# Optimization experiments

Measured on AMD Instinct MI355X. Metric: run time of the kernel, lower is better.

Reference implementation:

```python
import jax, jax.numpy as jnp
import numpy as np

N_NODES = 50000
N_GRAPHS = 64
D = 320


def gcn_conv(x, W, b, src, dst, n):
    # PyG GCNConv (default): add self loops, symmetric deg^-1/2 normalization,
    # linear transform, scatter-add aggregation at target, plus bias.
    h = x @ W  # [N, d_out]
    loop = jnp.arange(n)
    s = jnp.concatenate([src, loop])
    t = jnp.concatenate([dst, loop])
    deg = jax.ops.segment_sum(jnp.ones_like(t, dtype=h.dtype), t, num_segments=n)
    dinv = jnp.where(deg > 0, jax.lax.rsqrt(deg), 0.0)
    norm = dinv[s] * dinv[t]  # [E+N]
    msg = h[s] * norm[:, None]  # gather + scale, [E+N, d_out]
    out = jax.ops.segment_sum(msg, t, num_segments=n)
    return out + b


def setup_inputs() -> dict:
    key = jax.random.key(0)
    ks = jax.random.split(key, 12)
    x = jax.random.normal(ks[0], (N_NODES, D), dtype=jnp.float32)
    edge_index = jax.random.randint(ks[1], (2, 800000), 0, N_NODES, dtype=jnp.int64)
    batch = jnp.sort(jax.random.randint(ks[2], (N_NODES,), 0, N_GRAPHS, dtype=jnp.int64))

    def lin(k, fan_in, fan_out):
        bound = 1.0 / np.sqrt(fan_in)
        kw, kb = jax.random.split(k)
        W = jax.random.uniform(kw, (fan_in, fan_out), minval=-bound, maxval=bound, dtype=jnp.float32)
        b = jax.random.uniform(kb, (fan_out,), minval=-bound, maxval=bound, dtype=jnp.float32)
        return W, b

    W1, b1 = lin(ks[3], D, D)
    W2, b2 = lin(ks[4], D, D)
    W3, b3 = lin(ks[5], D, D)
    Wf1, bf1 = lin(ks[6], D, 256)
    Wf2, bf2 = lin(ks[7], 256, 16)
    Wf3, bf3 = lin(ks[8], 16, 1)
    return {"x": x, "W1": W1, "b1": b1, "W2": W2, "b2": b2, "W3": W3, "b3": b3,
            "Wf1": Wf1, "bf1": bf1, "Wf2": Wf2, "bf2": bf2, "Wf3": Wf3, "bf3": bf3,
            "edge_index": edge_index, "batch": batch}


def reference(x, W1, b1, W2, b2, W3, b3, Wf1, bf1, Wf2, bf2, Wf3, bf3, edge_index, batch):
    src, dst = edge_index[0], edge_index[1]
    n = x.shape[0]
    h = jax.nn.relu(gcn_conv(x, W1, b1, src, dst, n))
    h = jax.nn.relu(gcn_conv(h, W2, b2, src, dst, n))
    h = jax.nn.relu(gcn_conv(h, W3, b3, src, dst, n))
    g = jax.ops.segment_max(h, batch, num_segments=N_GRAPHS)  # global max pool [B, D]
    g = jax.nn.relu(g @ Wf1 + bf1)  # dropout is identity in eval mode
    g = jax.nn.relu(g @ Wf2 + bf2)
    return g @ Wf3 + bf3
```

## Files before the change

kernel.cpp:

```cpp
#include <hip/hip_runtime.h>
#include <hip/hip_bf16.h>

#define N_NODES 50000
#define N_EDGES 800000
#define N_GRAPHS 64
#define D 320
#define CAP 64
#define POOL_SPLIT 4

typedef __attribute__((ext_vector_type(8))) short s16x8;
typedef __attribute__((ext_vector_type(4))) float f32x4;
typedef __attribute__((ext_vector_type(4))) unsigned int u32x4;

__device__ inline ushort f2bf(float f) {
    __hip_bfloat16 h = __float2bfloat16(f);
    return *reinterpret_cast<ushort*>(&h);
}

__global__ __launch_bounds__(256) void k_cvt_w3(const float* __restrict__ W1,
                                                const float* __restrict__ W2,
                                                const float* __restrict__ W3,
                                                ushort* __restrict__ Wt) {
    int i = blockIdx.x * blockDim.x + threadIdx.x;
    if (i >= 3 * D * D) return;
    int w = i / (D * D), r = i % (D * D);
    const float* W = (w == 0) ? W1 : (w == 1) ? W2 : W3;
    int k = r / D, n = r % D;
    Wt[w * D * D + n * D + k] = f2bf(W[r]);
}

__global__ void k_fill(const int* __restrict__ src, const int* __restrict__ dst,
                       int* __restrict__ cursor, int* __restrict__ csr) {
    int e = blockIdx.x * blockDim.x + threadIdx.x;
    if (e < N_EDGES) {
        int d = dst[e];
        int p = atomicAdd(&cursor[d], 1);
        if (p < CAP) csr[d * CAP + p] = src[e];
    }
}

__global__ void k_dinv(const int* __restrict__ cursor, float* __restrict__ dinv) {
    int n = blockIdx.x * blockDim.x + threadIdx.x;
    if (n < N_NODES) dinv[n] = rsqrtf((float)(cursor[n] + 1));
}

#define GBM 128
#define GBK 32
#define LDK 40
template<int AMODE>
__global__ __launch_bounds__(512) void k_gemm(const void* __restrict__ Ain,
                                              const ushort* __restrict__ Wt,
                                              const float* __restrict__ dinv,
                                              ushort* __restrict__ P) {
    __shared__ ushort As[GBM][LDK];
    __shared__ ushort Bs[D][LDK];
    int t = threadIdx.x;
    int m0 = blockIdx.x * GBM;
    int lane = t & 63;
    int wid = t >> 6;
    int wm = wid & 1;
    int wn = wid >> 1;
    int r16 = lane & 15;
    int kb = (lane >> 4) * 8;

    f32x4 acc[4][5] = {};

    for (int k0 = 0; k0 < D; k0 += GBK) {
        #pragma unroll
        for (int u = 0; u < 4; ++u) {
            int gi = t + 512 * u;
            if (gi < 512) {
                int r = gi >> 2, s = gi & 3;
                int gr = m0 + r;
                s16x8 v = {};
                if (gr < N_NODES) {
                    int k = k0 + s * 8;
                    if constexpr (AMODE == 1) {
                        const float* Af = (const float*)Ain;
                        float4 a0 = *(const float4*)&Af[(size_t)gr * D + k];
                        float4 a1 = *(const float4*)&Af[(size_t)gr * D + k + 4];
                        v[0] = (short)f2bf(a0.x); v[1] = (short)f2bf(a0.y);
                        v[2] = (short)f2bf(a0.z); v[3] = (short)f2bf(a0.w);
                        v[4] = (short)f2bf(a1.x); v[5] = (short)f2bf(a1.y);
                        v[6] = (short)f2bf(a1.z); v[7] = (short)f2bf(a1.w);
                    } else {
                        const ushort* Ab = (const ushort*)Ain;
                        v = *(const s16x8*)&Ab[(size_t)gr * D + k];
                    }
                }
                *(s16x8*)&As[r][s * 8] = v;
            } else if (gi < 1792) {
                int gj = gi - 512;
                int r = gj >> 2, s = gj & 3;
                *(s16x8*)&Bs[r][s * 8] = *(const s16x8*)&Wt[(size_t)r * D + k0 + s * 8];
            }
        }
        __syncthreads();

        s16x8 af[4], bfr[5];
        #pragma unroll
        for (int mi = 0; mi < 4; ++mi)
            af[mi] = *(const s16x8*)&As[wm * 64 + mi * 16 + r16][kb];
        #pragma unroll
        for (int ni = 0; ni < 5; ++ni)
            bfr[ni] = *(const s16x8*)&Bs[wn * 80 + ni * 16 + r16][kb];
        #pragma unroll
        for (int mi = 0; mi < 4; ++mi)
            #pragma unroll
            for (int ni = 0; ni < 5; ++ni)
                acc[mi][ni] = __builtin_amdgcn_mfma_f32_16x16x32_bf16(af[mi], bfr[ni], acc[mi][ni], 0, 0, 0);
        __syncthreads();
    }

    #pragma unroll
    for (int mi = 0; mi < 4; ++mi) {
        int rbase = m0 + wm * 64 + mi * 16 + (lane >> 4) * 4;
        #pragma unroll
        for (int r = 0; r < 4; ++r) {
            int row = rbase + r;
            if (row < N_NODES) {
                float dv = dinv[row];
                #pragma unroll
                for (int ni = 0; ni < 5; ++ni) {
                    int col = wn * 80 + ni * 16 + r16;
                    P[(size_t)row * D + col] = f2bf(acc[mi][ni][r] * dv);
                }
            }
        }
    }
}

#define AGG_NPB 8
__global__ __launch_bounds__(320) void k_agg(const ushort* __restrict__ P,
                                             const int* __restrict__ cursor,
                                             const int* __restrict__ csr,
                                             const float* __restrict__ dinv,
                                             const float* __restrict__ bias,
                                             ushort* __restrict__ H) {
    int t = threadIdx.x;
    int nl = t / 40;
    int cg = t - nl * 40;
    int n  = blockIdx.x * AGG_NPB + nl;
    int c0 = cg * 8;
    size_t row = (size_t)n * D + c0;
    const char* Pb = (const char*)P;
    unsigned coff = (unsigned)(c0 * 2);

    f32x4 aE = {}, aO = {};
    {
        u32x4 u = *(const u32x4*)&P[row];
        aE += __builtin_bit_cast(f32x4, u << 16);
        aO += __builtin_bit_cast(f32x4, u & (unsigned int)0xffff0000u);
    }
    int deg = cursor[n];
    if (deg > CAP) deg = CAP;
    const int* lst = csr + n * CAP;
    int i = 0;
    for (; i + 4 <= deg; i += 4) {
        int s0 = lst[i], s1 = lst[i + 1], s2 = lst[i + 2], s3 = lst[i + 3];
        u32x4 u0 = *(const u32x4*)(Pb + (unsigned)s0 * (unsigned)(D * 2) + coff);
        u32x4 u1 = *(const u32x4*)(Pb + (unsigned)s1 * (unsigned)(D * 2) + coff);
        u32x4 u2 = *(const u32x4*)(Pb + (unsigned)s2 * (unsigned)(D * 2) + coff);
        u32x4 u3 = *(const u32x4*)(Pb + (unsigned)s3 * (unsigned)(D * 2) + coff);
        aE += __builtin_bit_cast(f32x4, u0 << 16);
        aO += __builtin_bit_cast(f32x4, u0 & (unsigned int)0xffff0000u);
        aE += __builtin_bit_cast(f32x4, u1 << 16);
        aO += __builtin_bit_cast(f32x4, u1 & (unsigned int)0xffff0000u);
        aE += __builtin_bit_cast(f32x4, u2 << 16);
        aO += __builtin_bit_cast(f32x4, u2 & (unsigned int)0xffff0000u);
        aE += __builtin_bit_cast(f32x4, u3 << 16);
        aO += __builtin_bit_cast(f32x4, u3 & (unsigned int)0xffff0000u);
    }
    for (; i < deg; ++i) {
        int s = lst[i];
        u32x4 u = *(const u32x4*)(Pb + (unsigned)s * (unsigned)(D * 2) + coff);
        aE += __builtin_bit_cast(f32x4, u << 16);
        aO += __builtin_bit_cast(f32x4, u & (unsigned int)0xffff0000u);
    }
    float dv = dinv[n];
    s16x8 ov;
    #pragma unroll
    for (int q = 0; q < 4; ++q) {
        float e = fmaxf(fmaf(dv, aE[q], bias[c0 + 2 * q]), 0.0f);
        float o = fmaxf(fmaf(dv, aO[q], bias[c0 + 2 * q + 1]), 0.0f);
        ov[2 * q]     = (short)f2bf(e);
        ov[2 * q + 1] = (short)f2bf(o);
    }
    *(s16x8*)&H[row] = ov;
}

__global__ __launch_bounds__(320) void k_pool(const ushort* __restrict__ H,
                                              const int* __restrict__ batch,
                                              float* __restrict__ Gp) {
    __shared__ int range[2];
    int sp = blockIdx.x;
    int b = blockIdx.y;
    int t = threadIdx.x;
    int nl = t / 40;
    int cg = t - nl * 40;
    int c0 = cg * 8;
    if (t < 2) {
        int target = b + t;
        int lo = 0, hi = N_NODES;
        while (lo < hi) {
            int mid = (lo + hi) >> 1;
            if (batch[mid] < target) lo = mid + 1; else hi = mid;
        }
        range[t] = lo;
    }
    __syncthreads();
    int s = range[0], e = range[1];
    f32x4 mE = {}, mO = {};
    for (int n = s + sp * 8 + nl; n < e; n += POOL_SPLIT * 8) {
        u32x4 u = *(const u32x4*)&H[(size_t)n * D + c0];
        f32x4 vE = __builtin_bit_cast(f32x4, u << 16);
        f32x4 vO = __builtin_bit_cast(f32x4, u & (unsigned int)0xffff0000u);
        #pragma unroll
        for (int q = 0; q < 4; ++q) {
            mE[q] = fmaxf(mE[q], vE[q]);
            mO[q] = fmaxf(mO[q], vO[q]);
        }
    }
    __shared__ float red[8][D];
    #pragma unroll
    for (int q = 0; q < 4; ++q) {
        red[nl][c0 + 2 * q]     = mE[q];
        red[nl][c0 + 2 * q + 1] = mO[q];
    }
    __syncthreads();
    if (nl == 0) {
        #pragma unroll
        for (int q = 0; q < 8; ++q) {
            int c = c0 + q;
            float m = red[0][c];
            #pragma unroll
            for (int r = 1; r < 8; ++r) m = fmaxf(m, red[r][c]);
            Gp[(sp * N_GRAPHS + b) * D + c] = m;
        }
    }
}

__global__ __launch_bounds__(256) void k_mlp(const float* __restrict__ Gp,
    const float* __restrict__ Wf1, const float* __restrict__ bf1,
    const float* __restrict__ Wf2, const float* __restrict__ bf2,
    const float* __restrict__ Wf3, const float* __restrict__ bf3,
    float* __restrict__ out) {
    __shared__ float g_s[D];
    __shared__ float s1[256];
    __shared__ float s2[16];
    int b = blockIdx.x;
    int t = threadIdx.x;
    for (int i = t; i < D; i += 256) {
        float m = Gp[b * D + i];
        #pragma unroll
        for (int sp = 1; sp < POOL_SPLIT; ++sp)
            m = fmaxf(m, Gp[(sp * N_GRAPHS + b) * D + i]);
        g_s[i] = m;
    }
    __syncthreads();
    float acc = bf1[t];
    for (int k = 0; k < D; ++k) acc = fmaf(g_s[k], Wf1[k * 256 + t], acc);
    s1[t] = fmaxf(acc, 0.0f);
    __syncthreads();
    if (t < 16) {
        float a2 = bf2[t];
        for (int k = 0; k < 256; ++k) a2 = fmaf(s1[k], Wf2[k * 16 + t], a2);
        s2[t] = fmaxf(a2, 0.0f);
    }
    __syncthreads();
    if (t == 0) {
        float a3 = bf3[0];
        #pragma unroll
        for (int k = 0; k < 16; ++k) a3 = fmaf(s2[k], Wf3[k], a3);
        out[b] = a3;
    }
}

extern "C" void kernel_launch(void* const* d_in, const int* in_sizes, int n_in,
                              void* d_out, int out_size, void* d_ws, size_t ws_size,
                              hipStream_t stream) {
    const float* x   = (const float*)d_in[0];
    const float* W1  = (const float*)d_in[1];
    const float* b1  = (const float*)d_in[2];
    const float* W2  = (const float*)d_in[3];
    const float* b2  = (const float*)d_in[4];
    const float* W3  = (const float*)d_in[5];
    const float* b3  = (const float*)d_in[6];
    const float* Wf1 = (const float*)d_in[7];
    const float* bf1 = (const float*)d_in[8];
    const float* Wf2 = (const float*)d_in[9];
    const float* bf2 = (const float*)d_in[10];
    const float* Wf3 = (const float*)d_in[11];
    const float* bf3 = (const float*)d_in[12];
    const int*   ei  = (const int*)d_in[13];
    const int*   src = ei;
    const int*   dst = ei + N_EDGES;
    const int*   batch = (const int*)d_in[14];
    float* out = (float*)d_out;

    char* p = (char*)d_ws;
    auto alloc = [&](size_t bytes) { char* r = p; p += (bytes + 255) & ~(size_t)255; return (void*)r; };
    const size_t NB = (size_t)N_NODES * D * sizeof(ushort);
    ushort* bB   = (ushort*)alloc(NB);
    ushort* bC   = (ushort*)alloc(NB);
    ushort* Wt   = (ushort*)alloc(3 * D * D * 2);
    float*  dinv = (float*)alloc(N_NODES * 4);
    int*    cursor = (int*)alloc(N_NODES * 4);
    int*    csr  = (int*)alloc((size_t)N_NODES * CAP * 4);
    float*  Gp   = (float*)alloc(POOL_SPLIT * N_GRAPHS * D * 4);

    hipMemsetAsync(cursor, 0, N_NODES * sizeof(int), stream);

    k_cvt_w3<<<(3 * D * D + 255) / 256, 256, 0, stream>>>(W1, W2, W3, Wt);

    k_fill<<<(N_EDGES + 255) / 256, 256, 0, stream>>>(src, dst, cursor, csr);
    k_dinv<<<(N_NODES + 255) / 256, 256, 0, stream>>>(cursor, dinv);

    int ggrid = (N_NODES + GBM - 1) / GBM;
    int agrid = N_NODES / AGG_NPB;
    k_gemm<1><<<ggrid, 512, 0, stream>>>(x, Wt, dinv, bB);
    k_agg<<<agrid, 320, 0, stream>>>(bB, cursor, csr, dinv, b1, bC);
    k_gemm<0><<<ggrid, 512, 0, stream>>>(bC, Wt + D * D, dinv, bB);
    k_agg<<<agrid, 320, 0, stream>>>(bB, cursor, csr, dinv, b2, bC);
    k_gemm<0><<<ggrid, 512, 0, stream>>>(bC, Wt + 2 * D * D, dinv, bB);
    k_agg<<<agrid, 320, 0, stream>>>(bB, cursor, csr, dinv, b3, bC);
    dim3 pgrid(POOL_SPLIT, N_GRAPHS);
    k_pool<<<pgrid, 320, 0, stream>>>(bC, batch, Gp);
    k_mlp<<<N_GRAPHS, 256, 0, stream>>>(Gp, Wf1, bf1, Wf2, bf2, Wf3, bf3, out);
}
```

Measured before the change: 395.0 us.

## Use direct global-to-LDS loads with XOR-style swizzle and fold dinv into consumers

The GEMM now loads the A (bf16 layers) and W tiles straight from global memory into LDS through global_load_lds, placed in a rotated-slot swizzle in place of padded rows. This removes the register round-trip and should avoid LDS bank conflicts. The separate dinv kernel and buffer are removed, and rsqrt(deg+1) is recomputed from cursor inside the GEMM epilogue and the aggregation kernel. The activation buffers are padded by one tile of rows so the unguarded direct loads past N_NODES stay in bounds, at the cost of reading garbage rows that are never stored.

```diff
diff --git a/kernel.cpp b/kernel.cpp
--- a/kernel.cpp
+++ b/kernel.cpp
@@ -15,6 +15,12 @@
 __device__ inline ushort f2bf(float f) {
     __hip_bfloat16 h = __float2bfloat16(f);
     return *reinterpret_cast<ushort*>(&h);
+}
+
+__device__ __forceinline__ void gload16(const void* g, void* l) {
+    __builtin_amdgcn_global_load_lds(
+        (const __attribute__((address_space(1))) unsigned int*)g,
+        (__attribute__((address_space(3))) unsigned int*)l, 16, 0, 0);
 }
 
 __global__ __launch_bounds__(256) void k_cvt_w3(const float* __restrict__ W1,
@@ -39,71 +45,74 @@
     }
 }
 
-__global__ void k_dinv(const int* __restrict__ cursor, float* __restrict__ dinv) {
-    int n = blockIdx.x * blockDim.x + threadIdx.x;
-    if (n < N_NODES) dinv[n] = rsqrtf((float)(cursor[n] + 1));
-}
-
 #define GBM 128
 #define GBK 32
-#define LDK 40
 template<int AMODE>
 __global__ __launch_bounds__(512) void k_gemm(const void* __restrict__ Ain,
                                               const ushort* __restrict__ Wt,
-                                              const float* __restrict__ dinv,
+                                              const int* __restrict__ cursor,
                                               ushort* __restrict__ P) {
-    __shared__ ushort As[GBM][LDK];
-    __shared__ ushort Bs[D][LDK];
+    __shared__ ushort As[GBM][GBK];
+    __shared__ ushort Bs[D][GBK];
     int t = threadIdx.x;
+    int lane = t & 63;
+    int w = t >> 6;
     int m0 = blockIdx.x * GBM;
-    int lane = t & 63;
-    int wid = t >> 6;
-    int wm = wid & 1;
-    int wn = wid >> 1;
+    int wm = w & 1;
+    int wn = w >> 1;
     int r16 = lane & 15;
-    int kb = (lane >> 4) * 8;
+    int tseg = lane >> 4;
+    int physsel = (tseg + (r16 >> 1)) & 3;
+
+    int agi = w * 64 + lane;
+    int ar = agi >> 2;
+    int asl = ((agi & 3) - (agi >> 3)) & 3;
+    char* AsWaveBase = (char*)As + w * 1024;
 
     f32x4 acc[4][5] = {};
 
     for (int k0 = 0; k0 < D; k0 += GBK) {
-        #pragma unroll
-        for (int u = 0; u < 4; ++u) {
-            int gi = t + 512 * u;
-            if (gi < 512) {
-                int r = gi >> 2, s = gi & 3;
-                int gr = m0 + r;
-                s16x8 v = {};
-                if (gr < N_NODES) {
-                    int k = k0 + s * 8;
-                    if constexpr (AMODE == 1) {
-                        const float* Af = (const float*)Ain;
-                        float4 a0 = *(const float4*)&Af[(size_t)gr * D + k];
-                        float4 a1 = *(const float4*)&Af[(size_t)gr * D + k + 4];
-                        v[0] = (short)f2bf(a0.x); v[1] = (short)f2bf(a0.y);
-                        v[2] = (short)f2bf(a0.z); v[3] = (short)f2bf(a0.w);
-                        v[4] = (short)f2bf(a1.x); v[5] = (short)f2bf(a1.y);
-                        v[6] = (short)f2bf(a1.z); v[7] = (short)f2bf(a1.w);
-                    } else {
-                        const ushort* Ab = (const ushort*)Ain;
-                        v = *(const s16x8*)&Ab[(size_t)gr * D + k];
-                    }
-                }
-                *(s16x8*)&As[r][s * 8] = v;
-            } else if (gi < 1792) {
-                int gj = gi - 512;
-                int r = gj >> 2, s = gj & 3;
-                *(s16x8*)&Bs[r][s * 8] = *(const s16x8*)&Wt[(size_t)r * D + k0 + s * 8];
+        if constexpr (AMODE == 0) {
+            const char* Ab = (const char*)Ain;
+            gload16(Ab + ((size_t)(m0 + ar) * D + k0 + asl * 8) * 2, AsWaveBase);
+        } else {
+            int gr = m0 + ar;
+            s16x8 v = {};
+            if (gr < N_NODES) {
+                const float* Af = (const float*)Ain;
+                const float* srcp = &Af[(size_t)gr * D + k0 + asl * 8];
+                float4 a0 = *(const float4*)srcp;
+                float4 a1 = *(const float4*)(srcp + 4);
+                v[0] = (short)f2bf(a0.x); v[1] = (short)f2bf(a0.y);
+                v[2] = (short)f2bf(a0.z); v[3] = (short)f2bf(a0.w);
+                v[4] = (short)f2bf(a1.x); v[5] = (short)f2bf(a1.y);
+                v[6] = (short)f2bf(a1.z); v[7] = (short)f2bf(a1.w);
             }
+            *(s16x8*)((char*)As + (size_t)agi * 16) = v;
+        }
+        #pragma unroll
+        for (int u = 0; u < 3; ++u) {
+            int gi = u * 512 + t;
+            if (gi < 1280) {
+                int r = gi >> 2;
+                int sl = ((gi & 3) - (gi >> 3)) & 3;
+                gload16((const char*)Wt + (size_t)r * (D * 2) + (size_t)(k0 + sl * 8) * 2,
+                        (char*)Bs + (size_t)(u * 512 + (t & ~63)) * 16);
+            }
         }
         __syncthreads();
 
         s16x8 af[4], bfr[5];
         #pragma unroll
-        for (int mi = 0; mi < 4; ++mi)
-            af[mi] = *(const s16x8*)&As[wm * 64 + mi * 16 + r16][kb];
-        #pragma unroll
-        for (int ni = 0; ni < 5; ++ni)
-            bfr[ni] = *(const s16x8*)&Bs[wn * 80 + ni * 16 + r16][kb];
+        for (int mi = 0; mi < 4; ++mi) {
+            int row = wm * 64 + mi * 16 + r16;
+            af[mi] = *(const s16x8*)((const char*)As + (size_t)row * 64 + physsel * 16);
+        }
+        #pragma unroll
+        for (int ni = 0; ni < 5; ++ni) {
+            int row = wn * 80 + ni * 16 + r16;
+            bfr[ni] = *(const s16x8*)((const char*)Bs + (size_t)row * 64 + physsel * 16);
+        }
         #pragma unroll
         for (int mi = 0; mi < 4; ++mi)
             #pragma unroll
@@ -119,7 +128,7 @@
         for (int r = 0; r < 4; ++r) {
             int row = rbase + r;
             if (row < N_NODES) {
-                float dv = dinv[row];
+                float dv = rsqrtf((float)(cursor[row] + 1));
                 #pragma unroll
                 for (int ni = 0; ni < 5; ++ni) {
                     int col = wn * 80 + ni * 16 + r16;
@@ -134,7 +143,6 @@
 __global__ __launch_bounds__(320) void k_agg(const ushort* __restrict__ P,
                                              const int* __restrict__ cursor,
                                              const int* __restrict__ csr,
-                                             const float* __restrict__ dinv,
                                              const float* __restrict__ bias,
                                              ushort* __restrict__ H) {
     int t = threadIdx.x;
@@ -152,8 +160,8 @@
         aE += __builtin_bit_cast(f32x4, u << 16);
         aO += __builtin_bit_cast(f32x4, u & (unsigned int)0xffff0000u);
     }
-    int deg = cursor[n];
-    if (deg > CAP) deg = CAP;
+    int cnt = cursor[n];
+    int deg = cnt > CAP ? CAP : cnt;
     const int* lst = csr + n * CAP;
     int i = 0;
     for (; i + 4 <= deg; i += 4) {
@@ -177,7 +185,7 @@
         aE += __builtin_bit_cast(f32x4, u << 16);
         aO += __builtin_bit_cast(f32x4, u & (unsigned int)0xffff0000u);
     }
-    float dv = dinv[n];
+    float dv = rsqrtf((float)(cnt + 1));
     s16x8 ov;
     #pragma unroll
     for (int q = 0; q < 4; ++q) {
@@ -300,11 +308,10 @@
 
     char* p = (char*)d_ws;
     auto alloc = [&](size_t bytes) { char* r = p; p += (bytes + 255) & ~(size_t)255; return (void*)r; };
-    const size_t NB = (size_t)N_NODES * D * sizeof(ushort);
-    ushort* bB   = (ushort*)alloc(NB);
-    ushort* bC   = (ushort*)alloc(NB);
+    const size_t NBP = (size_t)(N_NODES + GBM) * D * sizeof(ushort);
+    ushort* bB   = (ushort*)alloc(NBP);
+    ushort* bC   = (ushort*)alloc(NBP);
     ushort* Wt   = (ushort*)alloc(3 * D * D * 2);
-    float*  dinv = (float*)alloc(N_NODES * 4);
     int*    cursor = (int*)alloc(N_NODES * 4);
     int*    csr  = (int*)alloc((size_t)N_NODES * CAP * 4);
     float*  Gp   = (float*)alloc(POOL_SPLIT * N_GRAPHS * D * 4);
@@ -314,16 +321,15 @@
     k_cvt_w3<<<(3 * D * D + 255) / 256, 256, 0, stream>>>(W1, W2, W3, Wt);
 
     k_fill<<<(N_EDGES + 255) / 256, 256, 0, stream>>>(src, dst, cursor, csr);
-    k_dinv<<<(N_NODES + 255) / 256, 256, 0, stream>>>(cursor, dinv);
 
     int ggrid = (N_NODES + GBM - 1) / GBM;
     int agrid = N_NODES / AGG_NPB;
-    k_gemm<1><<<ggrid, 512, 0, stream>>>(x, Wt, dinv, bB);
-    k_agg<<<agrid, 320, 0, stream>>>(bB, cursor, csr, dinv, b1, bC);
-    k_gemm<0><<<ggrid, 512, 0, stream>>>(bC, Wt + D * D, dinv, bB);
-    k_agg<<<agrid, 320, 0, stream>>>(bB, cursor, csr, dinv, b2, bC);
-    k_gemm<0><<<ggrid, 512, 0, stream>>>(bC, Wt + 2 * D * D, dinv, bB);
-    k_agg<<<agrid, 320, 0, stream>>>(bB, cursor, csr, dinv, b3, bC);
+    k_gemm<1><<<ggrid, 512, 0, stream>>>(x, Wt, cursor, bB);
+    k_agg<<<agrid, 320, 0, stream>>>(bB, cursor, csr, b1, bC);
+    k_gemm<0><<<ggrid, 512, 0, stream>>>(bC, Wt + D * D, cursor, bB);
+    k_agg<<<agrid, 320, 0, stream>>>(bB, cursor, csr, b2, bC);
+    k_gemm<0><<<ggrid, 512, 0, stream>>>(bC, Wt + 2 * D * D, cursor, bB);
+    k_agg<<<agrid, 320, 0, stream>>>(bB, cursor, csr, b3, bC);
     dim3 pgrid(POOL_SPLIT, N_GRAPHS);
     k_pool<<<pgrid, 320, 0, stream>>>(bC, batch, Gp);
     k_mlp<<<N_GRAPHS, 256, 0, stream>>>(Gp, Wf1, bf1, Wf2, bf2, Wf3, bf3, out);
```

After: 406.0 us. +2.8%, slower.

## Fuse max-pool into last aggregation and fold memset and dinv into other kernels

Applied to the files above, without the earlier changes.

The global max pool now happens inside the final aggregation kernel. Each block reduces its 8 nodes per graph segment in shared memory and applies atomicMax on float bits to a zeroed G buffer, so the final H write and the separate pool kernel are no longer needed. The memset of cursor and the dinv kernel are removed: zeroing moves into the weight-conversion kernel, and rsqrt of the degree is recomputed inline in the gemm and aggregation kernels. This cuts launches and one full pass over H. The cost is atomic traffic, and the int atomicMax trick is valid only because post-ReLU values are non-negative.

```diff
diff --git a/kernel.cpp b/kernel.cpp
--- a/kernel.cpp
+++ b/kernel.cpp
@@ -6,7 +6,6 @@
 #define N_GRAPHS 64
 #define D 320
 #define CAP 64
-#define POOL_SPLIT 4
 
 typedef __attribute__((ext_vector_type(8))) short s16x8;
 typedef __attribute__((ext_vector_type(4))) float f32x4;
@@ -17,16 +16,21 @@
     return *reinterpret_cast<ushort*>(&h);
 }
 
-__global__ __launch_bounds__(256) void k_cvt_w3(const float* __restrict__ W1,
-                                                const float* __restrict__ W2,
-                                                const float* __restrict__ W3,
-                                                ushort* __restrict__ Wt) {
+__global__ __launch_bounds__(256) void k_prep(const float* __restrict__ W1,
+                                              const float* __restrict__ W2,
+                                              const float* __restrict__ W3,
+                                              ushort* __restrict__ Wt,
+                                              int* __restrict__ cursor,
+                                              float* __restrict__ G) {
     int i = blockIdx.x * blockDim.x + threadIdx.x;
-    if (i >= 3 * D * D) return;
-    int w = i / (D * D), r = i % (D * D);
-    const float* W = (w == 0) ? W1 : (w == 1) ? W2 : W3;
-    int k = r / D, n = r % D;
-    Wt[w * D * D + n * D + k] = f2bf(W[r]);
+    if (i < N_NODES) cursor[i] = 0;
+    if (i < N_GRAPHS * D) G[i] = 0.0f;
+    if (i < 3 * D * D) {
+        int w = i / (D * D), r = i % (D * D);
+        const float* W = (w == 0) ? W1 : (w == 1) ? W2 : W3;
+        int k = r / D, n = r % D;
+        Wt[w * D * D + n * D + k] = f2bf(W[r]);
+    }
 }
 
 __global__ void k_fill(const int* __restrict__ src, const int* __restrict__ dst,
@@ -39,18 +43,13 @@
     }
 }
 
-__global__ void k_dinv(const int* __restrict__ cursor, float* __restrict__ dinv) {
-    int n = blockIdx.x * blockDim.x + threadIdx.x;
-    if (n < N_NODES) dinv[n] = rsqrtf((float)(cursor[n] + 1));
-}
-
 #define GBM 128
 #define GBK 32
 #define LDK 40
 template<int AMODE>
 __global__ __launch_bounds__(512) void k_gemm(const void* __restrict__ Ain,
                                               const ushort* __restrict__ Wt,
-                                              const float* __restrict__ dinv,
+                                              const int* __restrict__ cursor,
                                               ushort* __restrict__ P) {
     __shared__ ushort As[GBM][LDK];
     __shared__ ushort Bs[D][LDK];
@@ -119,7 +118,7 @@
         for (int r = 0; r < 4; ++r) {
             int row = rbase + r;
             if (row < N_NODES) {
-                float dv = dinv[row];
+                float dv = rsqrtf((float)(cursor[row] + 1));
                 #pragma unroll
                 for (int ni = 0; ni < 5; ++ni) {
                     int col = wn * 80 + ni * 16 + r16;
@@ -131,12 +130,16 @@
 }
 
 #define AGG_NPB 8
+template<int POOL>
 __global__ __launch_bounds__(320) void k_agg(const ushort* __restrict__ P,
                                              const int* __restrict__ cursor,
                                              const int* __restrict__ csr,
-                                             const float* __restrict__ dinv,
                                              const float* __restrict__ bias,
-                                             ushort* __restrict__ H) {
+                                             ushort* __restrict__ H,
+                                             const int* __restrict__ batch,
+                                             float* __restrict__ G) {
+    __shared__ float red[AGG_NPB][D];
+    __shared__ int gid[AGG_NPB];
     int t = threadIdx.x;
     int nl = t / 40;
     int cg = t - nl * 40;
@@ -146,14 +149,16 @@
     const char* Pb = (const char*)P;
     unsigned coff = (unsigned)(c0 * 2);
 
+    if (POOL && t < AGG_NPB) gid[t] = (int)batch[blockIdx.x * AGG_NPB + t];
+
     f32x4 aE = {}, aO = {};
     {
         u32x4 u = *(const u32x4*)&P[row];
         aE += __builtin_bit_cast(f32x4, u << 16);
         aO += __builtin_bit_cast(f32x4, u & (unsigned int)0xffff0000u);
     }
-    int deg = cursor[n];
-    if (deg > CAP) deg = CAP;
+    int cnt = cursor[n];
+    int deg = cnt > CAP ? CAP : cnt;
     const int* lst = csr + n * CAP;
     int i = 0;
     for (; i + 4 <= deg; i += 4) {
@@ -177,70 +182,47 @@
         aE += __builtin_bit_cast(f32x4, u << 16);
         aO += __builtin_bit_cast(f32x4, u & (unsigned int)0xffff0000u);
     }
-    float dv = dinv[n];
-    s16x8 ov;
-    #pragma unroll
-    for (int q = 0; q < 4; ++q) {
-        float e = fmaxf(fmaf(dv, aE[q], bias[c0 + 2 * q]), 0.0f);
-        float o = fmaxf(fmaf(dv, aO[q], bias[c0 + 2 * q + 1]), 0.0f);
-        ov[2 * q]     = (short)f2bf(e);
-        ov[2 * q + 1] = (short)f2bf(o);
-    }
-    *(s16x8*)&H[row] = ov;
-}
-
-__global__ __launch_bounds__(320) void k_pool(const ushort* __restrict__ H,
-                                              const int* __restrict__ batch,
-                                              float* __restrict__ Gp) {
-    __shared__ int range[2];
-    int sp = blockIdx.x;
-    int b = blockIdx.y;
-    int t = threadIdx.x;
-    int nl = t / 40;
-    int cg = t - nl * 40;
-    int c0 = cg * 8;
-    if (t < 2) {
-        int target = b + t;
-        int lo = 0, hi = N_NODES;
-        while (lo < hi) {
-            int mid = (lo + hi) >> 1;
-            if (batch[mid] < target) lo = mid + 1; else hi = mid;
-        }
-        range[t] = lo;
-    }
-    __syncthreads();
-    int s = range[0], e = range[1];
-    f32x4 mE = {}, mO = {};
-    for (int n = s + sp * 8 + nl; n < e; n += POOL_SPLIT * 8) {
-        u32x4 u = *(const u32x4*)&H[(size_t)n * D + c0];
-        f32x4 vE = __builtin_bit_cast(f32x4, u << 16);
-        f32x4 vO = __builtin_bit_cast(f32x4, u & (unsigned int)0xffff0000u);
+    float dv = rsqrtf((float)(cnt + 1));
+
+    if constexpr (POOL == 0) {
+        s16x8 ov;
         #pragma unroll
         for (int q = 0; q < 4; ++q) {
-            mE[q] = fmaxf(mE[q], vE[q]);
-            mO[q] = fmaxf(mO[q], vO[q]);
-        }
-    }
-    __shared__ float red[8][D];
-    #pragma unroll
-    for (int q = 0; q < 4; ++q) {
-        red[nl][c0 + 2 * q]     = mE[q];
-        red[nl][c0 + 2 * q + 1] = mO[q];
-    }
-    __syncthreads();
-    if (nl == 0) {
-        #pragma unroll
-        for (int q = 0; q < 8; ++q) {
-            int c = c0 + q;
-            float m = red[0][c];
+            float e = fmaxf(fmaf(dv, aE[q], bias[c0 + 2 * q]), 0.0f);
+            float o = fmaxf(fmaf(dv, aO[q], bias[c0 + 2 * q + 1]), 0.0f);
+            ov[2 * q]     = (short)f2bf(e);
+            ov[2 * q + 1] = (short)f2bf(o);
+        }
+        *(s16x8*)&H[row] = ov;
+    } else {
+        #pragma unroll
+        for (int q = 0; q < 4; ++q) {
+            red[nl][c0 + 2 * q]     = fmaxf(fmaf(dv, aE[q], bias[c0 + 2 * q]), 0.0f);
+            red[nl][c0 + 2 * q + 1] = fmaxf(fmaf(dv, aO[q], bias[c0 + 2 * q + 1]), 0.0f);
+        }
+        __syncthreads();
+        if (nl == 0) {
             #pragma unroll
-            for (int r = 1; r < 8; ++r) m = fmaxf(m, red[r][c]);
-            Gp[(sp * N_GRAPHS + b) * D + c] = m;
-        }
-    }
-}
-
-__global__ __launch_bounds__(256) void k_mlp(const float* __restrict__ Gp,
+            for (int q = 0; q < 8; ++q) {
+                int c = c0 + q;
+                float m = red[0][c];
+                int g = gid[0];
+                #pragma unroll
+                for (int r = 1; r < AGG_NPB; ++r) {
+                    if (gid[r] == g) m = fmaxf(m, red[r][c]);
+                    else {
+                        atomicMax((int*)&G[g * D + c], __float_as_int(m));
+                        g = gid[r];
+                        m = red[r][c];
+                    }
+                }
+                atomicMax((int*)&G[g * D + c], __float_as_int(m));
+            }
+        }
+    }
+}
+
+__global__ __launch_bounds__(256) void k_mlp(const float* __restrict__ G,
     const float* __restrict__ Wf1, const float* __restrict__ bf1,
     const float* __restrict__ Wf2, const float* __restrict__ bf2,
     const float* __restrict__ Wf3, const float* __restrict__ bf3,
@@ -250,13 +232,7 @@
     __shared__ float s2[16];
     int b = blockIdx.x;
     int t = threadIdx.x;
-    for (int i = t; i < D; i += 256) {
-        float m = Gp[b * D + i];
-        #pragma unroll
-        for (int sp = 1; sp < POOL_SPLIT; ++sp)
-            m = fmaxf(m, Gp[(sp * N_GRAPHS + b) * D + i]);
-        g_s[i] = m;
-    }
+    for (int i = t; i < D; i += 256) g_s[i] = G[b * D + i];
     __syncthreads();
     float acc = bf1[t];
     for (int k = 0; k < D; ++k) acc = fmaf(g_s[k], Wf1[k * 256 + t], acc);
@@ -304,27 +280,20 @@
     ushort* bB   = (ushort*)alloc(NB);
     ushort* bC   = (ushort*)alloc(NB);
     ushort* Wt   = (ushort*)alloc(3 * D * D * 2);
-    float*  dinv = (float*)alloc(N_NODES * 4);
     int*    cursor = (int*)alloc(N_NODES * 4);
     int*    csr  = (int*)alloc((size_t)N_NODES * CAP * 4);
-    float*  Gp   = (float*)alloc(POOL_SPLIT * N_GRAPHS * D * 4);
-
-    hipMemsetAsync(cursor, 0, N_NODES * sizeof(int), stream);
-
-    k_cvt_w3<<<(3 * D * D + 255) / 256, 256, 0, stream>>>(W1, W2, W3, Wt);
-
+    float*  G    = (float*)alloc(N_GRAPHS * D * 4);
+
+    k_prep<<<(3 * D * D + 255) / 256, 256, 0, stream>>>(W1, W2, W3, Wt, cursor, G);
     k_fill<<<(N_EDGES + 255) / 256, 256, 0, stream>>>(src, dst, cursor, csr);
-    k_dinv<<<(N_NODES + 255) / 256, 256, 0, stream>>>(cursor, dinv);
 
     int ggrid = (N_NODES + GBM - 1) / GBM;
     int agrid = N_NODES / AGG_NPB;
-    k_gemm<1><<<ggrid, 512, 0, stream>>>(x, Wt, dinv, bB);
-    k_agg<<<agrid, 320, 0, stream>>>(bB, cursor, csr, dinv, b1, bC);
-    k_gemm<0><<<ggrid, 512, 0, stream>>>(bC, Wt + D * D, dinv, bB);
-    k_agg<<<agrid, 320, 0, stream>>>(bB, cursor, csr, dinv, b2, bC);
-    k_gemm<0><<<ggrid, 512, 0, stream>>>(bC, Wt + 2 * D * D, dinv, bB);
-    k_agg<<<agrid, 320, 0, stream>>>(bB, cursor, csr, dinv, b3, bC);
-    dim3 pgrid(POOL_SPLIT, N_GRAPHS);
-    k_pool<<<pgrid, 320, 0, stream>>>(bC, batch, Gp);
-    k_mlp<<<N_GRAPHS, 256, 0, stream>>>(Gp, Wf1, bf1, Wf2, bf2, Wf3, bf3, out);
-}
+    k_gemm<1><<<ggrid, 512, 0, stream>>>(x, Wt, cursor, bB);
+    k_agg<0><<<agrid, 320, 0, stream>>>(bB, cursor, csr, b1, bC, nullptr, nullptr);
+    k_gemm<0><<<ggrid, 512, 0, stream>>>(bC, Wt + D * D, cursor, bB);
+    k_agg<0><<<agrid, 320, 0, stream>>>(bB, cursor, csr, b2, bC, nullptr, nullptr);
+    k_gemm<0><<<ggrid, 512, 0, stream>>>(bC, Wt + 2 * D * D, cursor, bB);
+    k_agg<1><<<agrid, 320, 0, stream>>>(bB, cursor, csr, b3, nullptr, batch, G);
+    k_mlp<<<N_GRAPHS, 256, 0, stream>>>(G, Wf1, bf1, Wf2, bf2, Wf3, bf3, out);
+}
```

Result: slower. 413.9 us (+4.8%).
